# Kernel tuning notes

Hardware: AMD Instinct MI355X
Metric: run time of the kernel (lower is better)

## Reference

```python
import jax, jax.numpy as jnp
import numpy as np

B, S, HID = 16, 1, 2048
H, D = 32, 64
KV = 4096
SCALE = D ** -0.5


def setup_inputs() -> dict:
    key = jax.random.key(0)
    ks = jax.random.split(key, 5)
    x = jax.random.normal(ks[0], (B, S, HID), dtype=jnp.float32)
    bias = jax.random.normal(ks[1], (B, H, S, KV), dtype=jnp.float32)
    past_kv = jax.random.normal(ks[2], (2, B, H, KV, D), dtype=jnp.float32)
    # fused QKV projection weight: [3*H*D, hidden], no bias
    w_qkv = jax.random.normal(ks[3], (3 * H * D, HID), dtype=jnp.float32) * (HID ** -0.5)
    # output projection: [hidden, H*D]
    w_o = jax.random.normal(ks[4], (HID, H * D), dtype=jnp.float32) * (HID ** -0.5)
    return {"x": x, "bias": bias, "past_kv": past_kv, "w_qkv": w_qkv, "w_o": w_o}


def reference(x, bias, past_kv, w_qkv, w_o):
    # fused QKV projection: [B, S, 3*H*D]
    qkv = jnp.einsum('bsh,oh->bso', x, w_qkv)
    # -> [3, B, H, S, D]  (proj, heads interleaved as (proj heads head_dim))
    qkv = qkv.reshape(B, S, 3, H, D).transpose(2, 0, 3, 1, 4)
    q, k_new, v_new = qkv[0], qkv[1], qkv[2]
    # KV cache: keep first KV-1 entries, append current step's k/v as the last slot
    past_k = past_kv[0, :, :, : KV - 1]  # [B, H, KV-1, D]
    past_v = past_kv[1, :, :, : KV - 1]
    k = jnp.concatenate([past_k, k_new], axis=-2)  # [B, H, KV, D]
    v = jnp.concatenate([past_v, v_new], axis=-2)
    # SDPA with additive relative-position bias
    scores = jnp.einsum('bhqd,bhkd->bhqk', q, k) * SCALE + bias
    probs = jax.nn.softmax(scores, axis=-1)
    a = jnp.einsum('bhqk,bhkd->bhqd', probs, v)  # [B, H, S, D]
    a = a.transpose(0, 2, 1, 3).reshape(B, S, H * D)
    return jnp.einsum('bsf,of->bso', a, w_o)
```

## Files before the change

kernel.cpp:

```cpp
#include <hip/hip_runtime.h>
#include <math.h>

#define Bc     16
#define HIDc   2048
#define Hc     32
#define Dc     64
#define KVc    4096
#define QKVO   6144
#define SCALEc 0.125f
#define CHUNKS 4
#define CHUNK  1024

__global__ __launch_bounds__(256) void qkv_kernel(const float* __restrict__ x,
                                                  const float* __restrict__ w,
                                                  float* __restrict__ qkv) {
    __shared__ float4 xs[512];
    int blk = blockIdx.x;
    int b   = blk & 15;
    int og  = blk >> 4;
    int t = threadIdx.x, lane = t & 63, wid = t >> 6;
    const float4* xr = reinterpret_cast<const float4*>(x + (size_t)b * HIDc);
    xs[t]       = xr[t];
    xs[t + 256] = xr[t + 256];
    __syncthreads();
    int o0 = og * 64 + wid * 16;
#pragma unroll 2
    for (int i = 0; i < 16; ++i) {
        int o = o0 + i;
        const float4* wr = reinterpret_cast<const float4*>(w + (size_t)o * HIDc);
        float acc = 0.f;
#pragma unroll
        for (int j = 0; j < 8; ++j) {
            float4 a = xs[lane + 64 * j];
            float4 c = wr[lane + 64 * j];
            acc += a.x * c.x + a.y * c.y + a.z * c.z + a.w * c.w;
        }
#pragma unroll
        for (int off = 32; off >= 1; off >>= 1) acc += __shfl_xor(acc, off);
        if (lane == 0) qkv[(size_t)b * QKVO + o] = acc;
    }
}

__global__ __launch_bounds__(256, 4) void attn_chunk_kernel(const float* __restrict__ qkv,
                                                            const float* __restrict__ bias,
                                                            const float* __restrict__ past_kv,
                                                            float* __restrict__ part_o,
                                                            float* __restrict__ part_ms) {
    __shared__ float bs[CHUNK];
    __shared__ float accs[16][65];
    __shared__ float pm[16], ps[16];

    int blk = blockIdx.x;
    int c   = blk & (CHUNKS - 1);
    int bh  = blk >> 2;
    int h   = bh & 31;
    int b   = bh >> 5;
    int t    = threadIdx.x;
    int lane = t & 63;
    int wid  = t >> 6;
    int sg   = lane >> 4;
    int cg   = lane & 15;
    int row0 = c * CHUNK;

    reinterpret_cast<float4*>(bs)[t] =
        reinterpret_cast<const float4*>(bias + (size_t)bh * KVc + row0)[t];

    const float* qp = qkv + (size_t)b * QKVO + h * Dc;
    float4 q4 = reinterpret_cast<const float4*>(qp)[cg];

    const size_t kvstride = (size_t)KVc * Dc;
    const float* pastK = past_kv + (size_t)bh * kvstride + (size_t)row0 * Dc;
    const float* pastV = past_kv + (size_t)(Bc * Hc) * kvstride + (size_t)bh * kvstride
                         + (size_t)row0 * Dc;

    __syncthreads();

    int rbase = wid * 4 + sg;
    float m = -1e30f, s = 0.f;
    float4 acc = {0.f, 0.f, 0.f, 0.f};

    int nclean = (c == CHUNKS - 1) ? 7 : 8;
    for (int ot = 0; ot < nclean; ++ot) {
        int it = ot * 8;
        float4 k4[8], v4[8];
#pragma unroll
        for (int u = 0; u < 8; ++u) {
            int rl = (it + u) * 16 + rbase;
            k4[u] = reinterpret_cast<const float4*>(pastK + (size_t)rl * Dc)[cg];
        }
#pragma unroll
        for (int u = 0; u < 8; ++u) {
            int rl = (it + u) * 16 + rbase;
            v4[u] = reinterpret_cast<const float4*>(pastV + (size_t)rl * Dc)[cg];
        }
        float p[8];
#pragma unroll
        for (int u = 0; u < 8; ++u) {
            int rl = (it + u) * 16 + rbase;
            float pp = q4.x * k4[u].x + q4.y * k4[u].y + q4.z * k4[u].z + q4.w * k4[u].w;
            pp += __shfl_xor(pp, 1);
            pp += __shfl_xor(pp, 2);
            pp += __shfl_xor(pp, 4);
            pp += __shfl_xor(pp, 8);
            p[u] = fmaf(pp, SCALEc, bs[rl]);
        }
        float gm = p[0];
#pragma unroll
        for (int u = 1; u < 8; ++u) gm = fmaxf(gm, p[u]);
        float mn  = fmaxf(m, gm);
        float scl = __expf(m - mn);
        m = mn;
        float es = 0.f;
        float4 va = {0.f, 0.f, 0.f, 0.f};
#pragma unroll
        for (int u = 0; u < 8; ++u) {
            float e = __expf(p[u] - mn);
            es += e;
            va.x = fmaf(e, v4[u].x, va.x);
            va.y = fmaf(e, v4[u].y, va.y);
            va.z = fmaf(e, v4[u].z, va.z);
            va.w = fmaf(e, v4[u].w, va.w);
        }
        s = fmaf(s, scl, es);
        acc.x = fmaf(acc.x, scl, va.x);
        acc.y = fmaf(acc.y, scl, va.y);
        acc.z = fmaf(acc.z, scl, va.z);
        acc.w = fmaf(acc.w, scl, va.w);
    }
    if (c == CHUNKS - 1) {
        const float* knew = qkv + (size_t)b * QKVO + HIDc + h * Dc;
        const float* vnew = qkv + (size_t)b * QKVO + 2 * HIDc + h * Dc;
        int it = 56;
        float4 k4[8], v4[8];
#pragma unroll
        for (int u = 0; u < 8; ++u) {
            int rl = (it + u) * 16 + rbase;
            const float* kr = (rl == CHUNK - 1) ? knew : (pastK + (size_t)rl * Dc);
            k4[u] = reinterpret_cast<const float4*>(kr)[cg];
        }
#pragma unroll
        for (int u = 0; u < 8; ++u) {
            int rl = (it + u) * 16 + rbase;
            const float* vr = (rl == CHUNK - 1) ? vnew : (pastV + (size_t)rl * Dc);
            v4[u] = reinterpret_cast<const float4*>(vr)[cg];
        }
        float p[8];
#pragma unroll
        for (int u = 0; u < 8; ++u) {
            int rl = (it + u) * 16 + rbase;
            float pp = q4.x * k4[u].x + q4.y * k4[u].y + q4.z * k4[u].z + q4.w * k4[u].w;
            pp += __shfl_xor(pp, 1);
            pp += __shfl_xor(pp, 2);
            pp += __shfl_xor(pp, 4);
            pp += __shfl_xor(pp, 8);
            p[u] = fmaf(pp, SCALEc, bs[rl]);
        }
        float gm = p[0];
#pragma unroll
        for (int u = 1; u < 8; ++u) gm = fmaxf(gm, p[u]);
        float mn  = fmaxf(m, gm);
        float scl = __expf(m - mn);
        m = mn;
        float es = 0.f;
        float4 va = {0.f, 0.f, 0.f, 0.f};
#pragma unroll
        for (int u = 0; u < 8; ++u) {
            float e = __expf(p[u] - mn);
            es += e;
            va.x = fmaf(e, v4[u].x, va.x);
            va.y = fmaf(e, v4[u].y, va.y);
            va.z = fmaf(e, v4[u].z, va.z);
            va.w = fmaf(e, v4[u].w, va.w);
        }
        s = fmaf(s, scl, es);
        acc.x = fmaf(acc.x, scl, va.x);
        acc.y = fmaf(acc.y, scl, va.y);
        acc.z = fmaf(acc.z, scl, va.z);
        acc.w = fmaf(acc.w, scl, va.w);
    }

    int sgid = wid * 4 + sg;
    if (cg == 0) { pm[sgid] = m; ps[sgid] = s; }
    accs[sgid][cg * 4 + 0] = acc.x;
    accs[sgid][cg * 4 + 1] = acc.y;
    accs[sgid][cg * 4 + 2] = acc.z;
    accs[sgid][cg * 4 + 3] = acc.w;
    __syncthreads();
    if (t < 64) {
        float M = pm[0];
#pragma unroll
        for (int i = 1; i < 16; ++i) M = fmaxf(M, pm[i]);
        float S = 0.f, o = 0.f;
#pragma unroll
        for (int i = 0; i < 16; ++i) {
            float w = __expf(pm[i] - M);
            S += w * ps[i];
            o += w * accs[i][t];
        }
        part_o[((size_t)bh * CHUNKS + c) * Dc + t] = o;
        if (t == 0) {
            part_ms[((size_t)bh * CHUNKS + c) * 2 + 0] = M;
            part_ms[((size_t)bh * CHUNKS + c) * 2 + 1] = S;
        }
    }
}

__global__ __launch_bounds__(64) void attn_combine_kernel(const float* __restrict__ part_o,
                                                          const float* __restrict__ part_ms,
                                                          float* __restrict__ attn_out) {
    int bh = blockIdx.x;
    int d  = threadIdx.x;
    float mc[CHUNKS], sc_[CHUNKS];
#pragma unroll
    for (int c = 0; c < CHUNKS; ++c) {
        mc[c]  = part_ms[((size_t)bh * CHUNKS + c) * 2 + 0];
        sc_[c] = part_ms[((size_t)bh * CHUNKS + c) * 2 + 1];
    }
    float M = mc[0];
#pragma unroll
    for (int c = 1; c < CHUNKS; ++c) M = fmaxf(M, mc[c]);
    float S = 0.f, o = 0.f;
#pragma unroll
    for (int c = 0; c < CHUNKS; ++c) {
        float w = __expf(mc[c] - M);
        S += w * sc_[c];
        o += w * part_o[((size_t)bh * CHUNKS + c) * Dc + d];
    }
    attn_out[(size_t)bh * Dc + d] = o / S;
}

__global__ __launch_bounds__(256) void outproj_kernel(const float* __restrict__ attn,
                                                      const float* __restrict__ w_o,
                                                      float* __restrict__ out) {
    __shared__ float4 as[512];
    int blk = blockIdx.x;
    int b   = blk & 15;
    int fg  = blk >> 4;
    int t = threadIdx.x, lane = t & 63, wid = t >> 6;
    const float4* ar = reinterpret_cast<const float4*>(attn + (size_t)b * HIDc);
    as[t]       = ar[t];
    as[t + 256] = ar[t + 256];
    __syncthreads();
    int f0 = fg * 64 + wid * 16;
#pragma unroll 2
    for (int i = 0; i < 16; ++i) {
        int f = f0 + i;
        const float4* wr = reinterpret_cast<const float4*>(w_o + (size_t)f * HIDc);
        float acc = 0.f;
#pragma unroll
        for (int j = 0; j < 8; ++j) {
            float4 a = as[lane + 64 * j];
            float4 c = wr[lane + 64 * j];
            acc += a.x * c.x + a.y * c.y + a.z * c.z + a.w * c.w;
        }
#pragma unroll
        for (int off = 32; off >= 1; off >>= 1) acc += __shfl_xor(acc, off);
        if (lane == 0) out[(size_t)b * HIDc + f] = acc;
    }
}

extern "C" void kernel_launch(void* const* d_in, const int* in_sizes, int n_in,
                              void* d_out, int out_size, void* d_ws, size_t ws_size,
                              hipStream_t stream) {
    const float* x       = (const float*)d_in[0];
    const float* bias    = (const float*)d_in[1];
    const float* past_kv = (const float*)d_in[2];
    const float* w_qkv   = (const float*)d_in[3];
    const float* w_o     = (const float*)d_in[4];
    float* out = (float*)d_out;

    float* qkv     = (float*)d_ws;
    float* attn    = qkv + (size_t)Bc * QKVO;
    float* part_o  = attn + (size_t)Bc * HIDc;
    float* part_ms = part_o + (size_t)Bc * Hc * CHUNKS * Dc;

    qkv_kernel<<<dim3(Bc * (QKVO / 64)), dim3(256), 0, stream>>>(x, w_qkv, qkv);
    attn_chunk_kernel<<<dim3(Bc * Hc * CHUNKS), dim3(256), 0, stream>>>(qkv, bias, past_kv, part_o, part_ms);
    attn_combine_kernel<<<dim3(Bc * Hc), dim3(64), 0, stream>>>(part_o, part_ms, attn);
    outproj_kernel<<<dim3(Bc * (HIDc / 64)), dim3(256), 0, stream>>>(attn, w_o, out);
}
```

Before: 282.1 us.

## Batch all 16 rows per weight row in QKV and output projections

Rewrites the QKV and output projection GEMVs so each thread computes one output for one batch element. Each block covers 8 weight rows across all 16 batch rows, so every weight row is fetched from memory once rather than once per batch block. The price is per-thread sequential float4 reads along the row with limited coalescing inside a wave, and dropping the shared-memory staging and wave reductions.

```diff
diff --git a/kernel.cpp b/kernel.cpp
--- a/kernel.cpp
+++ b/kernel.cpp
@@ -11,34 +11,23 @@
 #define CHUNKS 4
 #define CHUNK  1024
 
-__global__ __launch_bounds__(256) void qkv_kernel(const float* __restrict__ x,
-                                                  const float* __restrict__ w,
-                                                  float* __restrict__ qkv) {
-    __shared__ float4 xs[512];
-    int blk = blockIdx.x;
-    int b   = blk & 15;
-    int og  = blk >> 4;
-    int t = threadIdx.x, lane = t & 63, wid = t >> 6;
+__global__ __launch_bounds__(128) void qkv_bat_kernel(const float* __restrict__ x,
+                                                      const float* __restrict__ w,
+                                                      float* __restrict__ qkv) {
+    int t = threadIdx.x;
+    int b = t & 15;
+    int r = t >> 4;
+    int row = blockIdx.x * 8 + r;
+    const float4* wr = reinterpret_cast<const float4*>(w + (size_t)row * HIDc);
     const float4* xr = reinterpret_cast<const float4*>(x + (size_t)b * HIDc);
-    xs[t]       = xr[t];
-    xs[t + 256] = xr[t + 256];
-    __syncthreads();
-    int o0 = og * 64 + wid * 16;
-#pragma unroll 2
-    for (int i = 0; i < 16; ++i) {
-        int o = o0 + i;
-        const float4* wr = reinterpret_cast<const float4*>(w + (size_t)o * HIDc);
-        float acc = 0.f;
-#pragma unroll
-        for (int j = 0; j < 8; ++j) {
-            float4 a = xs[lane + 64 * j];
-            float4 c = wr[lane + 64 * j];
-            acc += a.x * c.x + a.y * c.y + a.z * c.z + a.w * c.w;
-        }
-#pragma unroll
-        for (int off = 32; off >= 1; off >>= 1) acc += __shfl_xor(acc, off);
-        if (lane == 0) qkv[(size_t)b * QKVO + o] = acc;
-    }
+    float acc = 0.f;
+#pragma unroll 8
+    for (int c = 0; c < HIDc / 4; ++c) {
+        float4 a = wr[c];
+        float4 e = xr[c];
+        acc += a.x * e.x + a.y * e.y + a.z * e.z + a.w * e.w;
+    }
+    qkv[(size_t)b * QKVO + row] = acc;
 }
 
 __global__ __launch_bounds__(256, 4) void attn_chunk_kernel(const float* __restrict__ qkv,
@@ -229,34 +218,23 @@
     attn_out[(size_t)bh * Dc + d] = o / S;
 }
 
-__global__ __launch_bounds__(256) void outproj_kernel(const float* __restrict__ attn,
-                                                      const float* __restrict__ w_o,
-                                                      float* __restrict__ out) {
-    __shared__ float4 as[512];
-    int blk = blockIdx.x;
-    int b   = blk & 15;
-    int fg  = blk >> 4;
-    int t = threadIdx.x, lane = t & 63, wid = t >> 6;
+__global__ __launch_bounds__(128) void outproj_bat_kernel(const float* __restrict__ attn,
+                                                          const float* __restrict__ w_o,
+                                                          float* __restrict__ out) {
+    int t = threadIdx.x;
+    int b = t & 15;
+    int r = t >> 4;
+    int row = blockIdx.x * 8 + r;
+    const float4* wr = reinterpret_cast<const float4*>(w_o + (size_t)row * HIDc);
     const float4* ar = reinterpret_cast<const float4*>(attn + (size_t)b * HIDc);
-    as[t]       = ar[t];
-    as[t + 256] = ar[t + 256];
-    __syncthreads();
-    int f0 = fg * 64 + wid * 16;
-#pragma unroll 2
-    for (int i = 0; i < 16; ++i) {
-        int f = f0 + i;
-        const float4* wr = reinterpret_cast<const float4*>(w_o + (size_t)f * HIDc);
-        float acc = 0.f;
-#pragma unroll
-        for (int j = 0; j < 8; ++j) {
-            float4 a = as[lane + 64 * j];
-            float4 c = wr[lane + 64 * j];
-            acc += a.x * c.x + a.y * c.y + a.z * c.z + a.w * c.w;
-        }
-#pragma unroll
-        for (int off = 32; off >= 1; off >>= 1) acc += __shfl_xor(acc, off);
-        if (lane == 0) out[(size_t)b * HIDc + f] = acc;
-    }
+    float acc = 0.f;
+#pragma unroll 8
+    for (int c = 0; c < HIDc / 4; ++c) {
+        float4 a = wr[c];
+        float4 e = ar[c];
+        acc += a.x * e.x + a.y * e.y + a.z * e.z + a.w * e.w;
+    }
+    out[(size_t)b * HIDc + row] = acc;
 }
 
 extern "C" void kernel_launch(void* const* d_in, const int* in_sizes, int n_in,
@@ -274,8 +252,8 @@
     float* part_o  = attn + (size_t)Bc * HIDc;
     float* part_ms = part_o + (size_t)Bc * Hc * CHUNKS * Dc;
 
-    qkv_kernel<<<dim3(Bc * (QKVO / 64)), dim3(256), 0, stream>>>(x, w_qkv, qkv);
+    qkv_bat_kernel<<<dim3(QKVO / 8), dim3(128), 0, stream>>>(x, w_qkv, qkv);
     attn_chunk_kernel<<<dim3(Bc * Hc * CHUNKS), dim3(256), 0, stream>>>(qkv, bias, past_kv, part_o, part_ms);
     attn_combine_kernel<<<dim3(Bc * Hc), dim3(64), 0, stream>>>(part_o, part_ms, attn);
-    outproj_kernel<<<dim3(Bc * (HIDc / 64)), dim3(256), 0, stream>>>(attn, w_o, out);
-}
+    outproj_bat_kernel<<<dim3(HIDc / 8), dim3(128), 0, stream>>>(attn, w_o, out);
+}
```

New measurement: 364.5 us. 29.2% more time.
